# Kernel tuning notes

Hardware: AMD Instinct MI355X
Metric: run time of the kernel (lower is better)

Reference implementation:

```python
import jax, jax.numpy as jnp
import numpy as np

B, TQ, TK, D, DV = 8, 2048, 2048, 1024, 1024  # units == TK


def setup_inputs() -> dict:
    key = jax.random.key(0)
    kq, kk, kv, kb = jax.random.split(key, 4)
    q = jax.random.normal(kq, (B, TQ, D), dtype=jnp.float32)
    k = jax.random.normal(kk, (B, D, TK), dtype=jnp.float32)
    v = jax.random.normal(kv, (B, TK, DV), dtype=jnp.float32)
    b = 0.1 * jax.random.normal(kb, (TK,), dtype=jnp.float32)  # bias over key axis (units,)
    return {"q": q, "k": k, "v": v, "b": b}


def reference(q, k, v, b):
    # scores[b,i,j] = tanh(q_i . k_j + b_j)   -- additive-style biased dot scores
    scores = jnp.tanh(jnp.einsum("bqd,bdk->bqk", q, k) + b)  # [B, TQ, TK]
    # softmax over the key axis (axis=1 of the unbatched [TQ,TK] scores)
    weights = jax.nn.softmax(scores, axis=-1)
    # weighted sum of values
    context = jnp.einsum("bqk,bkv->bqv", weights, v)  # [B, TQ, DV]
    return context
```

## Files before the change

kernel.cpp:

```cpp
#include <hip/hip_runtime.h>
#include <hip/hip_bf16.h>
#include <stdint.h>

#define B_  8
#define TQ_ 2048
#define TK_ 2048
#define D_  1024
#define DV_ 1024

typedef __attribute__((ext_vector_type(8))) short  short8;
typedef __attribute__((ext_vector_type(4))) float  floatx4;

__device__ __forceinline__ void async_copy16(const void* g, void* l) {
  __builtin_amdgcn_global_load_lds(
      (const __attribute__((address_space(1))) unsigned int*)g,
      (__attribute__((address_space(3))) unsigned int*)l,
      16, 0, 0);
}

__device__ __forceinline__ ushort f2bf(float f) {
  union { __hip_bfloat16 b; ushort u; } cv;
  cv.b = __float2bfloat16(f);
  return cv.u;
}

__device__ __forceinline__ float bf2f(ushort u) {
  union { ushort u; __hip_bfloat16 b; } cv;
  cv.u = u;
  return __bfloat162float(cv.b);
}


__device__ __forceinline__ void transpose_body(const float* __restrict__ in,
                                               ushort* __restrict__ out,
                                               int R, int C, int r0, int c0,
                                               float (*tile)[65]) {
  const int t = threadIdx.x;
  {
    const int row = t >> 4, col = (t & 15) * 4;
    #pragma unroll
    for (int ro = 0; ro < 4; ro++) {
      const float4 f = *(const float4*)&in[(size_t)(r0 + ro * 16 + row) * C + c0 + col];
      tile[ro * 16 + row][col + 0] = f.x;
      tile[ro * 16 + row][col + 1] = f.y;
      tile[ro * 16 + row][col + 2] = f.z;
      tile[ro * 16 + row][col + 3] = f.w;
    }
  }
  __syncthreads();
  {
    const int c = t >> 4, rg = (t & 15) * 4;
    #pragma unroll
    for (int ro = 0; ro < 4; ro++) {
      const int cc = ro * 16 + c;
      ushort4 o;
      o.x = f2bf(tile[rg + 0][cc]);
      o.y = f2bf(tile[rg + 1][cc]);
      o.z = f2bf(tile[rg + 2][cc]);
      o.w = f2bf(tile[rg + 3][cc]);
      *(ushort4*)&out[(size_t)(c0 + cc) * R + r0 + rg] = o;
    }
  }
}

__global__ void prep(const float* __restrict__ q, const float* __restrict__ k,
                     const float* __restrict__ v, ushort* __restrict__ qb,
                     ushort* __restrict__ ktb, ushort* __restrict__ vtb) {
  __shared__ float tile[64][65];
  const int task = blockIdx.z >> 3;
  const int z    = blockIdx.z & 7;
  if (task == 0) {
    const float4* in  = (const float4*)(q + (size_t)z * TQ_ * D_);
    ushort4*      oup = (ushort4*)(qb + (size_t)z * TQ_ * D_);
    const int i0 = (blockIdx.y * 32 + blockIdx.x) * 1024 + threadIdx.x;
    #pragma unroll
    for (int it = 0; it < 4; it++) {
      const int i = i0 + it * 256;
      float4 f = in[i];
      ushort4 o;
      o.x = f2bf(f.x); o.y = f2bf(f.y); o.z = f2bf(f.z); o.w = f2bf(f.w);
      oup[i] = o;
    }
  } else if (task == 1) {
    transpose_body(k + (size_t)z * D_ * TK_, ktb + (size_t)z * TK_ * D_,
                   D_, TK_, blockIdx.y * 64, blockIdx.x * 64, tile);
  } else {
    transpose_body(v + (size_t)z * TK_ * DV_, vtb + (size_t)z * DV_ * TK_,
                   TK_, DV_, blockIdx.x * 64, blockIdx.y * 64, tile);
  }
}


#define WG_BARRIER() do { asm volatile("" ::: "memory");        \
                          __builtin_amdgcn_s_barrier();         \
                          asm volatile("" ::: "memory"); } while (0)
#define VMCNT(n) asm volatile("s_waitcnt vmcnt(" #n ")" ::: "memory")

__device__ __forceinline__ void stage128(const ushort* __restrict__ gp, int grow0,
                                         int k0, int KD, char* lds, int t) {
  const int rr  = t >> 3;
  const int s   = t & 7;
  const int gch = s ^ (rr & 7);
  const char* g0 = (const char*)(gp + (size_t)(grow0 + rr) * KD + k0) + gch * 16;
  async_copy16(g0, lds + t * 16);
  const char* g1 = (const char*)(gp + (size_t)(grow0 + 64 + rr) * KD + k0) + gch * 16;
  async_copy16(g1, lds + 8192 + t * 16);
}

template <int MH>
__device__ __forceinline__ void loadA(short8 (&a)[4][2], const char* Ab,
                                      int rowA, int off0, int off1) {
  #pragma unroll
  for (int j = 0; j < 4; ++j) {
    const char* p = Ab + rowA + (MH * 4 + j) * 2048;
    a[j][0] = *(const short8*)(p + off0);
    a[j][1] = *(const short8*)(p + off1);
  }
}

template <int NH>
__device__ __forceinline__ void loadB(short8 (&b)[2][2], const char* Bb,
                                      int rowB, int off0, int off1) {
  #pragma unroll
  for (int i = 0; i < 2; ++i) {
    const char* p = Bb + rowB + (NH * 2 + i) * 2048;
    b[i][0] = *(const short8*)(p + off0);
    b[i][1] = *(const short8*)(p + off1);
  }
}

template <int MH, int NH>
__device__ __forceinline__ void qmfma(floatx4 (&acc)[8][4], const short8 (&a)[4][2],
                                      const short8 (&b)[2][2]) {
  #pragma unroll
  for (int j = 0; j < 4; ++j)
    #pragma unroll
    for (int i = 0; i < 2; ++i) {
      floatx4 c = acc[MH * 4 + j][NH * 2 + i];
      c = __builtin_amdgcn_mfma_f32_16x16x32_bf16(a[j][0], b[i][0], c, 0, 0, 0);
      c = __builtin_amdgcn_mfma_f32_16x16x32_bf16(a[j][1], b[i][1], c, 0, 0, 0);
      acc[MH * 4 + j][NH * 2 + i] = c;
    }
}

template <int KDIM>
__device__ __forceinline__ void gemm_core8(const ushort* __restrict__ Ap,
                                           const ushort* __restrict__ Bp,
                                           char* lds, int bm0, int bn0,
                                           floatx4 (&acc)[8][4]) {
  const int t    = threadIdx.x;
  const int lane = t & 63;
  const int w    = t >> 6;
  const int wm   = w >> 2, wn = w & 3;
  const int lc   = lane & 15, q = lane >> 4;
  const int sw   = lc & 7;
  const int off0 = ((q)     ^ sw) * 16;
  const int off1 = ((4 + q) ^ sw) * 16;
  const int rowA = (wm * 128 + lc) * 128;
  const int rowB = (wn * 64  + lc) * 128;
  constexpr int NT = KDIM / 64;

  #pragma unroll
  for (int mi = 0; mi < 8; ++mi)
    #pragma unroll
    for (int ni = 0; ni < 4; ++ni)
      acc[mi][ni] = (floatx4){0.f, 0.f, 0.f, 0.f};

  char* A0b = lds;
  char* A1b = lds + 32768;
  char* B0b = lds + 65536;

  stage128(Ap, bm0,       0,  KDIM, A0b,         t);
  stage128(Ap, bm0 + 128, 0,  KDIM, A0b + 16384, t);
  stage128(Bp, bn0,       0,  KDIM, B0b,         t);
  stage128(Bp, bn0 + 128, 0,  KDIM, B0b + 16384, t);
  stage128(Ap, bm0,       64, KDIM, A1b,         t);
  stage128(Ap, bm0 + 128, 64, KDIM, A1b + 16384, t);
  VMCNT(4);
  WG_BARRIER();

  short8 a[4][2], b[2][2];
  #pragma unroll 2
  for (int tt = 0; tt < NT; ++tt) {
    char* Ab = lds + (tt & 1) * 32768;
    char* Bb = lds + 65536 + (tt & 1) * 32768;
    char* Bn = lds + 65536 + ((tt + 1) & 1) * 32768;

    loadA<0>(a, Ab, rowA, off0, off1);
    loadB<0>(b, Bb, rowB, off0, off1);
    if (tt + 1 < NT) {
      const int kb = (tt + 1) * 64;
      stage128(Bp, bn0,       kb, KDIM, Bn,         t);
      stage128(Bp, bn0 + 128, kb, KDIM, Bn + 16384, t);
    }
    WG_BARRIER();
    __builtin_amdgcn_s_setprio(1);
    qmfma<0, 0>(acc, a, b);
    __builtin_amdgcn_s_setprio(0);
    WG_BARRIER();

    loadB<1>(b, Bb, rowB, off0, off1);
    WG_BARRIER();
    __builtin_amdgcn_s_setprio(1);
    qmfma<0, 1>(acc, a, b);
    __builtin_amdgcn_s_setprio(0);
    WG_BARRIER();

    loadA<1>(a, Ab, rowA, off0, off1);
    WG_BARRIER();
    __builtin_amdgcn_s_setprio(1);
    qmfma<1, 1>(acc, a, b);
    __builtin_amdgcn_s_setprio(0);
    WG_BARRIER();

    loadB<0>(b, Bb, rowB, off0, off1);
    if (tt + 2 < NT) {
      const int ka = (tt + 2) * 64;
      stage128(Ap, bm0,       ka, KDIM, Ab,         t);
      stage128(Ap, bm0 + 128, ka, KDIM, Ab + 16384, t);
      VMCNT(4);
    } else {
      VMCNT(0);
    }
    WG_BARRIER();
    __builtin_amdgcn_s_setprio(1);
    qmfma<1, 0>(acc, a, b);
    __builtin_amdgcn_s_setprio(0);
    WG_BARRIER();
  }
}

__global__ __launch_bounds__(512, 2)
void gemm_qk(const ushort* __restrict__ Q, const ushort* __restrict__ Kt,
             const float* __restrict__ bias, ushort* __restrict__ P,
             float* __restrict__ lsum) {
  __shared__ short8 ldsv[8192];
  char* lds = (char*)ldsv;
  const int z   = blockIdx.z;
  const int bm0 = blockIdx.y * 256;
  const int bn0 = blockIdx.x * 256;

  floatx4 acc[8][4];
  gemm_core8<D_>(Q + (size_t)z * TQ_ * D_, Kt + (size_t)z * TK_ * D_,
                 lds, bm0, bn0, acc);

  const int lane = threadIdx.x & 63;
  const int w    = threadIdx.x >> 6;
  const int wm   = w >> 2, wn = w & 3;
  const int lc   = lane & 15, q = lane >> 4;
  ushort* Pb = P + (size_t)z * TQ_ * TK_;
  float*  lz = lsum + z * TQ_;

  #pragma unroll
  for (int mi = 0; mi < 8; ++mi) {
    const int grow = bm0 + wm * 128 + mi * 16 + (q << 2);
    float rs[4] = {0.f, 0.f, 0.f, 0.f};
    #pragma unroll
    for (int ni = 0; ni < 4; ++ni) {
      const int gcol = bn0 + wn * 64 + ni * 16 + lc;
      const float bj = bias[gcol];
      #pragma unroll
      for (int r = 0; r < 4; ++r) {
        float s = acc[mi][ni][r] + bj;
        float tnh = 1.f - 2.f / (__expf(2.f * s) + 1.f);
        float p   = __expf(tnh);
        ushort pu = f2bf(p);
        Pb[(size_t)(grow + r) * TK_ + gcol] = pu;
        rs[r] += bf2f(pu);
      }
    }
    #pragma unroll
    for (int r = 0; r < 4; ++r) {
      rs[r] += __shfl_xor(rs[r], 1, 64);
      rs[r] += __shfl_xor(rs[r], 2, 64);
      rs[r] += __shfl_xor(rs[r], 4, 64);
      rs[r] += __shfl_xor(rs[r], 8, 64);
    }
    if (lc == 0) {
      #pragma unroll
      for (int r = 0; r < 4; ++r) atomicAdd(&lz[grow + r], rs[r]);
    }
  }
}

__global__ __launch_bounds__(512, 2)
void gemm_pv(const ushort* __restrict__ P, const ushort* __restrict__ Vt,
             const float* __restrict__ lsum, float* __restrict__ out) {
  __shared__ short8 ldsv[8192];
  char* lds = (char*)ldsv;
  const int z   = blockIdx.z;
  const int bm0 = blockIdx.y * 256;
  const int bn0 = blockIdx.x * 256;

  floatx4 acc[8][4];
  gemm_core8<TK_>(P + (size_t)z * TQ_ * TK_, Vt + (size_t)z * DV_ * TK_,
                  lds, bm0, bn0, acc);

  const int lane = threadIdx.x & 63;
  const int w    = threadIdx.x >> 6;
  const int wm   = w >> 2, wn = w & 3;
  const int lc   = lane & 15, q = lane >> 4;
  float* ob = out + (size_t)z * TQ_ * DV_;
  const float* lz = lsum + z * TQ_;

  #pragma unroll
  for (int mi = 0; mi < 8; ++mi) {
    const int grow = bm0 + wm * 128 + mi * 16 + (q << 2);
    float linv[4];
    #pragma unroll
    for (int r = 0; r < 4; ++r) linv[r] = 1.f / lz[grow + r];
    #pragma unroll
    for (int ni = 0; ni < 4; ++ni) {
      const int gcol = bn0 + wn * 64 + ni * 16 + lc;
      #pragma unroll
      for (int r = 0; r < 4; ++r)
        ob[(size_t)(grow + r) * DV_ + gcol] = acc[mi][ni][r] * linv[r];
    }
  }
}


extern "C" void kernel_launch(void* const* d_in, const int* in_sizes, int n_in,
                              void* d_out, int out_size, void* d_ws, size_t ws_size,
                              hipStream_t stream) {
  const float* q    = (const float*)d_in[0];
  const float* k    = (const float*)d_in[1];
  const float* v    = (const float*)d_in[2];
  const float* bias = (const float*)d_in[3];
  float* out = (float*)d_out;

  char* ws = (char*)d_ws;
  ushort* qb   = (ushort*)(ws);
  ushort* ktb  = (ushort*)(ws + 33554432);
  ushort* vtb  = (ushort*)(ws + 67108864);
  ushort* P    = (ushort*)(ws + 100663296);
  float*  lsum = (float*)(ws + 167772160);

  hipMemsetAsync(lsum, 0, B_ * TQ_ * sizeof(float), stream);

  prep<<<dim3(32, 16, 24), dim3(256), 0, stream>>>(q, k, v, qb, ktb, vtb);

  gemm_qk<<<dim3(TK_ / 256, TQ_ / 256, B_), dim3(512), 0, stream>>>(qb, ktb, bias, P, lsum);
  gemm_pv<<<dim3(DV_ / 256, TQ_ / 256, B_), dim3(512), 0, stream>>>(P, vtb, lsum, out);
}
```

Before: 379.1 us.

## Restructure GEMM pipeline into k-half LDS stages with XCD-aware block remapping

Rewrites the shared GEMM core so each 64-wide k tile is staged as two 32-wide halves with a new swizzle and finer-grained async copies. The MFMA schedule becomes four 4x4 phases that interleave next-tile A/B prefetches with rolling k offsets. It also remaps workgroup indices so consecutive tiles land on the same XCD, aiming for better L2 reuse. The rolling wraparound offsets prefetch useless data past the end, and the tighter vmcnt accounting must be exactly right to stay correct.

```diff
diff --git a/kernel.cpp b/kernel.cpp
--- a/kernel.cpp
+++ b/kernel.cpp
@@ -29,7 +29,6 @@
   cv.u = u;
   return __bfloat162float(cv.b);
 }
-
 
 __device__ __forceinline__ void transpose_body(const float* __restrict__ in,
                                                ushort* __restrict__ out,
@@ -96,53 +95,6 @@
                           asm volatile("" ::: "memory"); } while (0)
 #define VMCNT(n) asm volatile("s_waitcnt vmcnt(" #n ")" ::: "memory")
 
-__device__ __forceinline__ void stage128(const ushort* __restrict__ gp, int grow0,
-                                         int k0, int KD, char* lds, int t) {
-  const int rr  = t >> 3;
-  const int s   = t & 7;
-  const int gch = s ^ (rr & 7);
-  const char* g0 = (const char*)(gp + (size_t)(grow0 + rr) * KD + k0) + gch * 16;
-  async_copy16(g0, lds + t * 16);
-  const char* g1 = (const char*)(gp + (size_t)(grow0 + 64 + rr) * KD + k0) + gch * 16;
-  async_copy16(g1, lds + 8192 + t * 16);
-}
-
-template <int MH>
-__device__ __forceinline__ void loadA(short8 (&a)[4][2], const char* Ab,
-                                      int rowA, int off0, int off1) {
-  #pragma unroll
-  for (int j = 0; j < 4; ++j) {
-    const char* p = Ab + rowA + (MH * 4 + j) * 2048;
-    a[j][0] = *(const short8*)(p + off0);
-    a[j][1] = *(const short8*)(p + off1);
-  }
-}
-
-template <int NH>
-__device__ __forceinline__ void loadB(short8 (&b)[2][2], const char* Bb,
-                                      int rowB, int off0, int off1) {
-  #pragma unroll
-  for (int i = 0; i < 2; ++i) {
-    const char* p = Bb + rowB + (NH * 2 + i) * 2048;
-    b[i][0] = *(const short8*)(p + off0);
-    b[i][1] = *(const short8*)(p + off1);
-  }
-}
-
-template <int MH, int NH>
-__device__ __forceinline__ void qmfma(floatx4 (&acc)[8][4], const short8 (&a)[4][2],
-                                      const short8 (&b)[2][2]) {
-  #pragma unroll
-  for (int j = 0; j < 4; ++j)
-    #pragma unroll
-    for (int i = 0; i < 2; ++i) {
-      floatx4 c = acc[MH * 4 + j][NH * 2 + i];
-      c = __builtin_amdgcn_mfma_f32_16x16x32_bf16(a[j][0], b[i][0], c, 0, 0, 0);
-      c = __builtin_amdgcn_mfma_f32_16x16x32_bf16(a[j][1], b[i][1], c, 0, 0, 0);
-      acc[MH * 4 + j][NH * 2 + i] = c;
-    }
-}
-
 template <int KDIM>
 __device__ __forceinline__ void gemm_core8(const ushort* __restrict__ Ap,
                                            const ushort* __restrict__ Bp,
@@ -153,12 +105,27 @@
   const int w    = t >> 6;
   const int wm   = w >> 2, wn = w & 3;
   const int lc   = lane & 15, q = lane >> 4;
-  const int sw   = lc & 7;
-  const int off0 = ((q)     ^ sw) * 16;
-  const int off1 = ((4 + q) ^ sw) * 16;
-  const int rowA = (wm * 128 + lc) * 128;
-  const int rowB = (wn * 64  + lc) * 128;
+  const int offq = (q ^ ((lc >> 1) & 3)) * 16;
   constexpr int NT = KDIM / 64;
+
+  const char* Abase = lds + (wm * 128 + lc) * 64 + offq;
+  const char* Bbase = lds + 65536 + (wn * 64 + lc) * 64 + offq;
+
+  const int srow = t >> 2;
+  const int sch  = (t & 3) ^ ((t >> 3) & 3);
+  const ushort* gA = Ap + (size_t)(bm0 + srow) * KDIM + sch * 8;
+  const ushort* gB = Bp + (size_t)(bn0 + srow) * KDIM + sch * 8;
+
+  auto stageA = [&](int buf, int kh, int kb) {
+    char* d = lds + buf * 32768 + kh * 16384 + t * 16;
+    async_copy16(gA + kb, d);
+    async_copy16(gA + (size_t)128 * KDIM + kb, d + 8192);
+  };
+  auto stageB = [&](int buf, int kh, int kb) {
+    char* d = lds + 65536 + buf * 32768 + kh * 16384 + t * 16;
+    async_copy16(gB + kb, d);
+    async_copy16(gB + (size_t)128 * KDIM + kb, d + 8192);
+  };
 
   #pragma unroll
   for (int mi = 0; mi < 8; ++mi)
@@ -166,68 +133,92 @@
     for (int ni = 0; ni < 4; ++ni)
       acc[mi][ni] = (floatx4){0.f, 0.f, 0.f, 0.f};
 
-  char* A0b = lds;
-  char* A1b = lds + 32768;
-  char* B0b = lds + 65536;
-
-  stage128(Ap, bm0,       0,  KDIM, A0b,         t);
-  stage128(Ap, bm0 + 128, 0,  KDIM, A0b + 16384, t);
-  stage128(Bp, bn0,       0,  KDIM, B0b,         t);
-  stage128(Bp, bn0 + 128, 0,  KDIM, B0b + 16384, t);
-  stage128(Ap, bm0,       64, KDIM, A1b,         t);
-  stage128(Ap, bm0 + 128, 64, KDIM, A1b + 16384, t);
-  VMCNT(4);
+  stageB(0, 0, 0);   stageA(0, 0, 0);
+  stageB(0, 1, 32);  stageA(0, 1, 32);
+  stageB(1, 0, 64);  stageA(1, 0, 64);
+  stageB(1, 1, 96);
+  VMCNT(10);
   WG_BARRIER();
 
-  short8 a[4][2], b[2][2];
+  int kA1 = 96, kB0 = 128, kA0 = 128, kB1 = 160;
+
+  short8 a[4], b0[4], b1[4];
   #pragma unroll 2
   for (int tt = 0; tt < NT; ++tt) {
-    char* Ab = lds + (tt & 1) * 32768;
-    char* Bb = lds + 65536 + (tt & 1) * 32768;
-    char* Bn = lds + 65536 + ((tt + 1) & 1) * 32768;
-
-    loadA<0>(a, Ab, rowA, off0, off1);
-    loadB<0>(b, Bb, rowB, off0, off1);
-    if (tt + 1 < NT) {
-      const int kb = (tt + 1) * 64;
-      stage128(Bp, bn0,       kb, KDIM, Bn,         t);
-      stage128(Bp, bn0 + 128, kb, KDIM, Bn + 16384, t);
-    }
+    const int cur = tt & 1, nxt = cur ^ 1;
+    const char* A  = Abase + cur * 32768;
+    const char* Bq = Bbase + cur * 32768;
+
+    #pragma unroll
+    for (int j = 0; j < 4; ++j) a[j]  = *(const short8*)(A + j * 1024);
+    #pragma unroll
+    for (int i = 0; i < 4; ++i) b0[i] = *(const short8*)(Bq + i * 1024);
+    stageA(nxt, 1, kA1); kA1 += 64; if (kA1 >= KDIM) kA1 -= KDIM;
     WG_BARRIER();
     __builtin_amdgcn_s_setprio(1);
-    qmfma<0, 0>(acc, a, b);
+    #pragma unroll
+    for (int j = 0; j < 4; ++j)
+      #pragma unroll
+      for (int i = 0; i < 4; ++i)
+        acc[j][i] = __builtin_amdgcn_mfma_f32_16x16x32_bf16(a[j], b0[i], acc[j][i], 0, 0, 0);
     __builtin_amdgcn_s_setprio(0);
     WG_BARRIER();
 
-    loadB<1>(b, Bb, rowB, off0, off1);
+    #pragma unroll
+    for (int j = 0; j < 4; ++j) a[j] = *(const short8*)(A + 4096 + j * 1024);
+    stageB(cur, 0, kB0); kB0 += 64; if (kB0 >= KDIM) kB0 -= KDIM;
+    VMCNT(10);
     WG_BARRIER();
     __builtin_amdgcn_s_setprio(1);
-    qmfma<0, 1>(acc, a, b);
+    #pragma unroll
+    for (int j = 0; j < 4; ++j)
+      #pragma unroll
+      for (int i = 0; i < 4; ++i)
+        acc[4 + j][i] = __builtin_amdgcn_mfma_f32_16x16x32_bf16(a[j], b0[i], acc[4 + j][i], 0, 0, 0);
     __builtin_amdgcn_s_setprio(0);
     WG_BARRIER();
 
-    loadA<1>(a, Ab, rowA, off0, off1);
+    #pragma unroll
+    for (int j = 0; j < 4; ++j) a[j]  = *(const short8*)(A + 16384 + j * 1024);
+    #pragma unroll
+    for (int i = 0; i < 4; ++i) b1[i] = *(const short8*)(Bq + 16384 + i * 1024);
+    stageA(cur, 0, kA0); kA0 += 64; if (kA0 >= KDIM) kA0 -= KDIM;
     WG_BARRIER();
     __builtin_amdgcn_s_setprio(1);
-    qmfma<1, 1>(acc, a, b);
+    #pragma unroll
+    for (int j = 0; j < 4; ++j)
+      #pragma unroll
+      for (int i = 0; i < 4; ++i)
+        acc[j][i] = __builtin_amdgcn_mfma_f32_16x16x32_bf16(a[j], b1[i], acc[j][i], 0, 0, 0);
     __builtin_amdgcn_s_setprio(0);
     WG_BARRIER();
 
-    loadB<0>(b, Bb, rowB, off0, off1);
-    if (tt + 2 < NT) {
-      const int ka = (tt + 2) * 64;
-      stage128(Ap, bm0,       ka, KDIM, Ab,         t);
-      stage128(Ap, bm0 + 128, ka, KDIM, Ab + 16384, t);
-      VMCNT(4);
-    } else {
-      VMCNT(0);
-    }
+    #pragma unroll
+    for (int j = 0; j < 4; ++j) a[j] = *(const short8*)(A + 16384 + 4096 + j * 1024);
+    stageB(cur, 1, kB1); kB1 += 64; if (kB1 >= KDIM) kB1 -= KDIM;
+    VMCNT(8);
     WG_BARRIER();
     __builtin_amdgcn_s_setprio(1);
-    qmfma<1, 0>(acc, a, b);
+    #pragma unroll
+    for (int j = 0; j < 4; ++j)
+      #pragma unroll
+      for (int i = 0; i < 4; ++i)
+        acc[4 + j][i] = __builtin_amdgcn_mfma_f32_16x16x32_bf16(a[j], b1[i], acc[4 + j][i], 0, 0, 0);
     __builtin_amdgcn_s_setprio(0);
     WG_BARRIER();
   }
+  VMCNT(0);
+}
+
+__device__ __forceinline__ void xcd_coords(int& bx, int& by, int& bz) {
+  const int gx = gridDim.x, gy = gridDim.y;
+  int lidx = blockIdx.x + gx * (blockIdx.y + gy * blockIdx.z);
+  const int nwg = gx * gy * gridDim.z;
+  lidx = (lidx & 7) * (nwg >> 3) + (lidx >> 3);
+  bx = lidx % gx;
+  const int byz = lidx / gx;
+  by = byz % gy;
+  bz = byz / gy;
 }
 
 __global__ __launch_bounds__(512, 2)
@@ -236,9 +227,10 @@
              float* __restrict__ lsum) {
   __shared__ short8 ldsv[8192];
   char* lds = (char*)ldsv;
-  const int z   = blockIdx.z;
-  const int bm0 = blockIdx.y * 256;
-  const int bn0 = blockIdx.x * 256;
+  int bx, by, z;
+  xcd_coords(bx, by, z);
+  const int bm0 = by * 256;
+  const int bn0 = bx * 256;
 
   floatx4 acc[8][4];
   gemm_core8<D_>(Q + (size_t)z * TQ_ * D_, Kt + (size_t)z * TK_ * D_,
@@ -288,9 +280,10 @@
              const float* __restrict__ lsum, float* __restrict__ out) {
   __shared__ short8 ldsv[8192];
   char* lds = (char*)ldsv;
-  const int z   = blockIdx.z;
-  const int bm0 = blockIdx.y * 256;
-  const int bn0 = blockIdx.x * 256;
+  int bx, by, z;
+  xcd_coords(bx, by, z);
+  const int bm0 = by * 256;
+  const int bn0 = bx * 256;
 
   floatx4 acc[8][4];
   gemm_core8<TK_>(P + (size_t)z * TQ_ * TK_, Vt + (size_t)z * DV_ * TK_,
```

Measured after the change: 382.8 us. No clear change (+1.0%).
